# Kernel tuning notes

Measured on AMD Instinct MI355X. Metric: run time of the kernel, lower is better.

The kernel has to match this reference:

```python
import jax, jax.numpy as jnp
import numpy as np

EPS = 1e-9
NEG = -99.0


def setup_inputs() -> dict:
    key = jax.random.key(0)
    k1, k2 = jax.random.split(key)
    N, D, LEN_PRD = 8192, 512, 4096
    embeddings = jax.random.normal(k1, (N, D), dtype=jnp.float32)
    W = jax.random.randint(k2, (N, N), 0, 2, dtype=jnp.int32)
    return {"embeddings": embeddings, "W": W, "len_prd": LEN_PRD, "head": 1}


def reference(embeddings, W, len_prd, head):
    # mask = -99 * (1 - W_block)
    Wb = (W[:len_prd, len_prd:] if head == 1 else W).astype(jnp.float32)
    mask = NEG * (1.0 - Wb)

    # row-normalize embeddings with eps clamp on norms
    norms = jnp.linalg.norm(embeddings, axis=1, keepdims=True)
    norms = jnp.where(norms <= EPS, EPS, norms)
    ne = embeddings / norms

    # cosine similarity; when head==1 only the [:len_prd, len_prd:] block is
    # kept, so compute just that block (same math as full matmul + slice)
    if head == 1:
        sim = ne[:len_prd] @ ne[len_prd:].T  # [len_prd, N-len_prd]
    else:
        sim = ne @ ne.T

    masked = sim + mask

    # output_matrix = clamp(relu(masked), max=1)
    output_matrix = jnp.minimum(jnp.maximum(masked, 0.0), 1.0)

    # half_normalized = 1 / (1 - masked); row-sum normalize with eps clamp
    half = 1.0 / (1.0 - masked)
    row_sum = jnp.sum(half, axis=1, keepdims=True)
    row_sum = jnp.where(row_sum <= EPS, EPS, row_sum)
    normed = half / row_sum

    # supple flag: 1 if no positive entry in the masked row, else 0;
    # zero out flagged rows and append the flag as an extra column
    supple = jnp.where(jnp.any(masked > 0.0, axis=1), 0.0, 1.0)  # [x_len]
    processed = jnp.where(supple[:, None] == 1.0, 0.0, normed)
    extended = jnp.concatenate([processed, supple[:, None]], axis=1)

    return (output_matrix, extended)
```

## Files before the change

kernel.cpp:

```cpp
#include <hip/hip_runtime.h>
#include <hip/hip_bf16.h>
#include <stdint.h>

#define NROW 8192
#define DIM  512
#define LP   4096
#define NB   4096
#define EXTW 4097
#define NEGC (-99.0f)
#define EPSF 1e-9f

typedef __attribute__((ext_vector_type(8))) __bf16 bf16x8;
typedef __attribute__((ext_vector_type(4))) float f32x4;

__global__ __launch_bounds__(256) void k_norm(const float* __restrict__ emb,
                                              __hip_bfloat16* __restrict__ ne) {
    const int row = blockIdx.x;
    const int t = threadIdx.x;
    const float* rp = emb + (size_t)row * DIM;
    float2 v = *(const float2*)(rp + t * 2);
    float s = v.x * v.x + v.y * v.y;
    #pragma unroll
    for (int off = 32; off; off >>= 1) s += __shfl_down(s, off);
    __shared__ float wsum[4];
    const int wid = t >> 6, lane = t & 63;
    if (lane == 0) wsum[wid] = s;
    __syncthreads();
    float tot = wsum[0] + wsum[1] + wsum[2] + wsum[3];
    float nrm = sqrtf(tot);
    nrm = (nrm <= EPSF) ? EPSF : nrm;
    const float inv = 1.0f / nrm;
    __hip_bfloat162 pk;
    pk.x = __float2bfloat16(v.x * inv);
    pk.y = __float2bfloat16(v.y * inv);
    *(__hip_bfloat162*)(ne + (size_t)row * DIM + t * 2) = pk;
}

#define BM 128
#define BN 128
#define BK 64
#define SIMLD 132

#define GLOAD_LDS(gp, lp) __builtin_amdgcn_global_load_lds(                     \
    (const __attribute__((address_space(1))) uint32_t*)(gp),                    \
    (__attribute__((address_space(3))) uint32_t*)(lp), 16, 0, 0)

__global__ __launch_bounds__(256) void k_gemm(const __hip_bfloat16* __restrict__ ne,
                                              const int* __restrict__ W,
                                              float* __restrict__ out0,
                                              float* __restrict__ ext) {
    __shared__ __align__(16) char smem[32768];
    __bf16* As = (__bf16*)smem;
    __bf16* Bs = (__bf16*)(smem + 16384);
    float*  Sim = (float*)smem;

    const int bid = blockIdx.x;
    const int wg = (bid & 7) * 128 + (bid >> 3);
    const int tileR = wg >> 5, tileC = wg & 31;

    const int tid = threadIdx.x;
    const int lane = tid & 63, wid = tid >> 6;
    const int wr = wid >> 1, wc = wid & 1;
    const int r16 = lane & 15, kg = lane >> 4;

    const __bf16* A = (const __bf16*)ne + (size_t)(tileR * BM) * DIM;
    const __bf16* B = (const __bf16*)ne + (size_t)(LP + tileC * BN) * DIM;

    const int srow = lane >> 3;
    const int scol = (lane & 7) * 8;

    f32x4 acc[4][4] = {};

    for (int kt = 0; kt < 8; ++kt) {
        const int k0 = kt * BK;
        #pragma unroll
        for (int i = 0; i < 4; ++i) {
            const int seg = wid * 4 + i;
            const int r = seg * 8 + srow;
            GLOAD_LDS(A + (size_t)r * DIM + k0 + scol, As + seg * 512);
            GLOAD_LDS(B + (size_t)r * DIM + k0 + scol, Bs + seg * 512);
        }
        __syncthreads();
        #pragma unroll
        for (int kk = 0; kk < 2; ++kk) {
            bf16x8 af[4], bfr[4];
            #pragma unroll
            for (int m = 0; m < 4; ++m)
                af[m] = *(const bf16x8*)(As + (wr * 64 + m * 16 + r16) * 64 + kk * 32 + kg * 8);
            #pragma unroll
            for (int n = 0; n < 4; ++n)
                bfr[n] = *(const bf16x8*)(Bs + (wc * 64 + n * 16 + r16) * 64 + kk * 32 + kg * 8);
            #pragma unroll
            for (int m = 0; m < 4; ++m)
                #pragma unroll
                for (int n = 0; n < 4; ++n)
                    acc[m][n] = __builtin_amdgcn_mfma_f32_16x16x32_bf16(af[m], bfr[n], acc[m][n], 0, 0, 0);
        }
        __syncthreads();
    }

    const int gr_base = tileR * BM;
    const int gc_base = tileC * BN;
    const int lr = (tid >> 5);
    const int cc = (tid & 31) * 4;

    int4 wreg[2][4];
    auto LOADW = [&](int m, int4 (&wq)[4]) {
        #pragma unroll
        for (int p = 0; p < 4; ++p) {
            const int r = p * 8 + lr;
            const int gr = gr_base + ((r >> 4) << 6) + m * 16 + (r & 15);
            wq[p] = *(const int4*)(W + (size_t)gr * NROW + LP + gc_base + cc);
        }
    };

    LOADW(0, wreg[0]);
    #pragma unroll
    for (int m = 0; m < 4; ++m) {
        __syncthreads();
        #pragma unroll
        for (int n = 0; n < 4; ++n)
            #pragma unroll
            for (int j = 0; j < 4; ++j)
                Sim[(wr * 16 + kg * 4 + j) * SIMLD + wc * 64 + n * 16 + r16] = acc[m][n][j];
        if (m < 3) LOADW(m + 1, wreg[(m + 1) & 1]);
        __syncthreads();
        #pragma unroll
        for (int p = 0; p < 4; ++p) {
            const int r = p * 8 + lr;
            const int gr = gr_base + ((r >> 4) << 6) + m * 16 + (r & 15);
            const int gc = gc_base + cc;
            const float4 s4 = *(const float4*)(Sim + r * SIMLD + cc);
            const int4 w4 = wreg[m & 1][p];
            const float m0 = w4.x ? s4.x : (s4.x + NEGC);
            const float m1 = w4.y ? s4.y : (s4.y + NEGC);
            const float m2 = w4.z ? s4.z : (s4.z + NEGC);
            const float m3 = w4.w ? s4.w : (s4.w + NEGC);
            float4 o;
            o.x = fminf(fmaxf(m0, 0.0f), 1.0f);
            o.y = fminf(fmaxf(m1, 0.0f), 1.0f);
            o.z = fminf(fmaxf(m2, 0.0f), 1.0f);
            o.w = fminf(fmaxf(m3, 0.0f), 1.0f);
            *(float4*)(out0 + (size_t)gr * NB + gc) = o;
            float* ex = ext + (size_t)gr * EXTW + gc;
            ex[0] = 1.0f / (1.0f - m0);
            ex[1] = 1.0f / (1.0f - m1);
            ex[2] = 1.0f / (1.0f - m2);
            ex[3] = 1.0f / (1.0f - m3);
        }
    }
}

__global__ __launch_bounds__(256) void k_final(float* __restrict__ ext) {
    const int row = blockIdx.x;
    float* rp = ext + (size_t)row * EXTW;
    const int t = threadIdx.x;
    float v[16];
    float s = 0.0f;
    int any = 0;
    #pragma unroll
    for (int i = 0; i < 16; ++i) {
        v[i] = rp[t + i * 256];
        s += v[i];
        any |= (v[i] > 1.0f) ? 1 : 0;
    }
    #pragma unroll
    for (int off = 32; off; off >>= 1) {
        s += __shfl_down(s, off);
        any |= __shfl_down(any, off);
    }
    __shared__ float ss[4];
    __shared__ int sa[4];
    const int wid = t >> 6, lane = t & 63;
    if (lane == 0) { ss[wid] = s; sa[wid] = any; }
    __syncthreads();
    float tot = ss[0] + ss[1] + ss[2] + ss[3];
    const int anyt = sa[0] | sa[1] | sa[2] | sa[3];
    tot = (tot <= EPSF) ? EPSF : tot;
    const float inv = anyt ? (1.0f / tot) : 0.0f;
    #pragma unroll
    for (int i = 0; i < 16; ++i) rp[t + i * 256] = v[i] * inv;
    if (t == 0) rp[NB] = anyt ? 0.0f : 1.0f;
}

extern "C" void kernel_launch(void* const* d_in, const int* in_sizes, int n_in,
                              void* d_out, int out_size, void* d_ws, size_t ws_size,
                              hipStream_t stream) {
    const float* emb = (const float*)d_in[0];
    const int* W = (const int*)d_in[1];

    float* out0 = (float*)d_out;
    float* ext = (float*)d_out + (size_t)LP * NB;
    __hip_bfloat16* ne = (__hip_bfloat16*)d_ws;

    k_norm<<<dim3(NROW), dim3(256), 0, stream>>>(emb, ne);
    k_gemm<<<dim3((LP / BM) * (NB / BN)), dim3(256), 0, stream>>>(ne, W, out0, ext);
    k_final<<<dim3(LP), dim3(256), 0, stream>>>(ext);
}
```

Before: 85.05 us.

## Process two column tiles per block, overlapping first tile's epilogue with second GEMM

Each GEMM workgroup now computes two adjacent 128x128 output tiles. The masked epilogue of the first tile (W loads, out0 and ext stores) is interleaved into the k-loop of the second tile's MFMA computation, using a separate LDS region for the Sim staging buffer. This aims to hide epilogue memory traffic behind matrix math. In exchange the grid is halved to 512 blocks, which is fewer than two per CU on a 256-CU part, register pressure rises with two accumulator sets, and LDS usage grows to about 48KB.

Result: slower. 92.63 us (+8.9%).

```diff
diff --git a/kernel.cpp b/kernel.cpp
--- a/kernel.cpp
+++ b/kernel.cpp
@@ -49,14 +49,16 @@
                                               const int* __restrict__ W,
                                               float* __restrict__ out0,
                                               float* __restrict__ ext) {
-    __shared__ __align__(16) char smem[32768];
+    __shared__ __align__(16) char smem[49664];
     __bf16* As = (__bf16*)smem;
     __bf16* Bs = (__bf16*)(smem + 16384);
-    float*  Sim = (float*)smem;
+    float*  Sim = (float*)(smem + 32768);
 
     const int bid = blockIdx.x;
-    const int wg = (bid & 7) * 128 + (bid >> 3);
-    const int tileR = wg >> 5, tileC = wg & 31;
+    const int wg = (bid & 7) * 64 + (bid >> 3);
+    const int tileR = wg >> 4;
+    const int tileC0 = (wg & 15) * 2;
+    const int tileC1 = tileC0 + 1;
 
     const int tid = threadIdx.x;
     const int lane = tid & 63, wid = tid >> 6;
@@ -64,23 +66,24 @@
     const int r16 = lane & 15, kg = lane >> 4;
 
     const __bf16* A = (const __bf16*)ne + (size_t)(tileR * BM) * DIM;
-    const __bf16* B = (const __bf16*)ne + (size_t)(LP + tileC * BN) * DIM;
+    const __bf16* B0 = (const __bf16*)ne + (size_t)(LP + tileC0 * BN) * DIM;
+    const __bf16* B1 = (const __bf16*)ne + (size_t)(LP + tileC1 * BN) * DIM;
 
     const int srow = lane >> 3;
     const int scol = (lane & 7) * 8;
 
-    f32x4 acc[4][4] = {};
-
-    for (int kt = 0; kt < 8; ++kt) {
+    auto STAGE = [&](const __bf16* Bp, int kt) {
         const int k0 = kt * BK;
         #pragma unroll
         for (int i = 0; i < 4; ++i) {
             const int seg = wid * 4 + i;
             const int r = seg * 8 + srow;
             GLOAD_LDS(A + (size_t)r * DIM + k0 + scol, As + seg * 512);
-            GLOAD_LDS(B + (size_t)r * DIM + k0 + scol, Bs + seg * 512);
-        }
-        __syncthreads();
+            GLOAD_LDS(Bp + (size_t)r * DIM + k0 + scol, Bs + seg * 512);
+        }
+    };
+
+    auto MFMA_STEP = [&](f32x4 (&acc)[4][4]) {
         #pragma unroll
         for (int kk = 0; kk < 2; ++kk) {
             bf16x8 af[4], bfr[4];
@@ -96,42 +99,36 @@
                 for (int n = 0; n < 4; ++n)
                     acc[m][n] = __builtin_amdgcn_mfma_f32_16x16x32_bf16(af[m], bfr[n], acc[m][n], 0, 0, 0);
         }
-        __syncthreads();
-    }
+    };
 
     const int gr_base = tileR * BM;
-    const int gc_base = tileC * BN;
     const int lr = (tid >> 5);
     const int cc = (tid & 31) * 4;
 
     int4 wreg[2][4];
-    auto LOADW = [&](int m, int4 (&wq)[4]) {
+    auto LOADW = [&](int gcb, int m, int4 (&wq)[4]) {
         #pragma unroll
         for (int p = 0; p < 4; ++p) {
             const int r = p * 8 + lr;
             const int gr = gr_base + ((r >> 4) << 6) + m * 16 + (r & 15);
-            wq[p] = *(const int4*)(W + (size_t)gr * NROW + LP + gc_base + cc);
-        }
-    };
-
-    LOADW(0, wreg[0]);
-    #pragma unroll
-    for (int m = 0; m < 4; ++m) {
-        __syncthreads();
+            wq[p] = *(const int4*)(W + (size_t)gr * NROW + LP + gcb + cc);
+        }
+    };
+    auto SIMW = [&](f32x4 (&acc)[4][4], int m) {
         #pragma unroll
         for (int n = 0; n < 4; ++n)
             #pragma unroll
             for (int j = 0; j < 4; ++j)
                 Sim[(wr * 16 + kg * 4 + j) * SIMLD + wc * 64 + n * 16 + r16] = acc[m][n][j];
-        if (m < 3) LOADW(m + 1, wreg[(m + 1) & 1]);
-        __syncthreads();
+    };
+    auto STORES = [&](int gcb, int m, int4 (&wq)[4]) {
         #pragma unroll
         for (int p = 0; p < 4; ++p) {
             const int r = p * 8 + lr;
             const int gr = gr_base + ((r >> 4) << 6) + m * 16 + (r & 15);
-            const int gc = gc_base + cc;
+            const int gc = gcb + cc;
             const float4 s4 = *(const float4*)(Sim + r * SIMLD + cc);
-            const int4 w4 = wreg[m & 1][p];
+            const int4 w4 = wq[p];
             const float m0 = w4.x ? s4.x : (s4.x + NEGC);
             const float m1 = w4.y ? s4.y : (s4.y + NEGC);
             const float m2 = w4.z ? s4.z : (s4.z + NEGC);
@@ -148,6 +145,44 @@
             ex[2] = 1.0f / (1.0f - m2);
             ex[3] = 1.0f / (1.0f - m3);
         }
+    };
+
+    const int gcb0 = tileC0 * BN;
+    const int gcb1 = tileC1 * BN;
+
+    f32x4 acc0[4][4] = {};
+    #pragma unroll
+    for (int kt = 0; kt < 8; ++kt) {
+        STAGE(B0, kt);
+        __syncthreads();
+        MFMA_STEP(acc0);
+        __syncthreads();
+    }
+
+    f32x4 acc1[4][4] = {};
+    LOADW(gcb0, 0, wreg[0]);
+    #pragma unroll
+    for (int kt = 0; kt < 8; ++kt) {
+        STAGE(B1, kt);
+        if ((kt & 1) == 0) SIMW(acc0, kt >> 1);
+        __syncthreads();
+        if ((kt & 1) == 0) {
+            const int c = kt >> 1;
+            if (c < 3) LOADW(gcb0, c + 1, wreg[(c + 1) & 1]);
+            STORES(gcb0, c, wreg[c & 1]);
+        }
+        MFMA_STEP(acc1);
+        __syncthreads();
+    }
+
+    LOADW(gcb1, 0, wreg[0]);
+    #pragma unroll
+    for (int m = 0; m < 4; ++m) {
+        __syncthreads();
+        SIMW(acc1, m);
+        if (m < 3) LOADW(gcb1, m + 1, wreg[(m + 1) & 1]);
+        __syncthreads();
+        STORES(gcb1, m, wreg[m & 1]);
     }
 }
 
@@ -194,6 +229,6 @@
     __hip_bfloat16* ne = (__hip_bfloat16*)d_ws;
 
     k_norm<<<dim3(NROW), dim3(256), 0, stream>>>(emb, ne);
-    k_gemm<<<dim3((LP / BM) * (NB / BN)), dim3(256), 0, stream>>>(ne, W, out0, ext);
+    k_gemm<<<dim3(512), dim3(256), 0, stream>>>(ne, W, out0, ext);
     k_final<<<dim3(LP), dim3(256), 0, stream>>>(ext);
 }
```
